# Kernel optimization log

Measured on AMD Instinct MI355X. Metric: run time of the kernel, lower is better.

## Reference

```python
import jax, jax.numpy as jnp
import numpy as np

N_NODES = 64000
N_GRAPHS = 128


def _sage_conv(x, edge_index, Wl, Wr, b):
    # PyG SAGEConv (mean aggregator): out = lin_l(mean_{j in N(i)} x_j) + lin_r(x_i)
    src, dst = edge_index[0], edge_index[1]
    msg = x[src]                                   # [E, d] gather
    s = jax.ops.segment_sum(msg, dst, num_segments=N_NODES)          # [N, d]
    cnt = jax.ops.segment_sum(jnp.ones(src.shape, x.dtype), dst,
                              num_segments=N_NODES)[:, None]          # [N, 1]
    aggr = jnp.where(cnt > 0, s / jnp.maximum(cnt, 1.0), jnp.zeros((), x.dtype))
    return aggr @ Wl.T + x @ Wr.T + b


def setup_inputs() -> dict:
    key = jax.random.key(0)
    ks = jax.random.split(key, 9)
    E = 1024000
    x = jax.random.normal(ks[0], (N_NODES, 64), dtype=jnp.float32)
    edge_index = jax.random.randint(ks[1], (2, E), 0, N_NODES, dtype=jnp.int64)
    batch = jnp.sort(jax.random.randint(ks[2], (N_NODES,), 0, N_GRAPHS, dtype=jnp.int64))
    sc = 1.0 / np.sqrt(64.0)
    Wl = jax.random.normal(ks[3], (3, 64, 64), dtype=jnp.float32) * sc
    Wr = jax.random.normal(ks[4], (3, 64, 64), dtype=jnp.float32) * sc
    b = jax.random.normal(ks[5], (3, 64), dtype=jnp.float32) * sc
    Wl_out = jax.random.normal(ks[6], (2, 64), dtype=jnp.float32) * sc
    Wr_out = jax.random.normal(ks[7], (2, 64), dtype=jnp.float32) * sc
    b_out = jax.random.normal(ks[8], (2,), dtype=jnp.float32) * sc
    return {"x": x, "edge_index": edge_index, "batch": batch,
            "Wl": Wl, "Wr": Wr, "b": b,
            "Wl_out": Wl_out, "Wr_out": Wr_out, "b_out": b_out}


def reference(x, edge_index, batch, Wl, Wr, b, Wl_out, Wr_out, b_out):
    h = x
    for i in range(Wl.shape[0]):  # fixed n_layers=3 hidden SAGEConv layers
        h = _sage_conv(h, edge_index, Wl[i], Wr[i], b[i])
        # dropout is identity at inference
        h = jax.nn.relu(h)
    h = _sage_conv(h, edge_index, Wl_out, Wr_out, b_out)  # [N, n_classes]
    # global mean pool over graphs in the batch
    s = jax.ops.segment_sum(h, batch, num_segments=N_GRAPHS)
    cnt = jax.ops.segment_sum(jnp.ones((N_NODES,), h.dtype), batch,
                              num_segments=N_GRAPHS)[:, None]
    return s / jnp.maximum(cnt, 1.0)
```

## Files before the change

### kernel.cpp

```cpp
#include <hip/hip_runtime.h>

#define NNODES 64000
#define NGRAPHS 128
#define D 64
#define NT 250
#define ESEG 5120
#define ZG 1024

typedef _Float16 half8 __attribute__((ext_vector_type(8)));
typedef float f32x4 __attribute__((ext_vector_type(4)));

__device__ __forceinline__ int lower_bound(const int* __restrict__ a, int n, int key) {
    int lo = 0, hi = n;
    while (lo < hi) {
        int mid = (lo + hi) >> 1;
        if (a[mid] < key) lo = mid + 1; else hi = mid;
    }
    return lo;
}


__global__ void tohalf_kernel(const float4* __restrict__ x, half8* __restrict__ xh, int n8,
                              const float* __restrict__ Wl, const float* __restrict__ Wr,
                              _Float16* __restrict__ Wlh, _Float16* __restrict__ Wrh,
                              int* __restrict__ ecur, float* __restrict__ pool) {
    int i = blockIdx.x * blockDim.x + threadIdx.x;
    int st = gridDim.x * blockDim.x;
    for (; i < n8; i += st) {
        float4 a = x[2 * i], b = x[2 * i + 1];
        half8 o;
        o[0] = (_Float16)a.x; o[1] = (_Float16)a.y; o[2] = (_Float16)a.z; o[3] = (_Float16)a.w;
        o[4] = (_Float16)b.x; o[5] = (_Float16)b.y; o[6] = (_Float16)b.z; o[7] = (_Float16)b.w;
        xh[i] = o;
    }
    int j = blockIdx.x * blockDim.x + threadIdx.x;
    if (j < 3 * D * D) {
        Wlh[j] = (_Float16)Wl[j];
        Wrh[j] = (_Float16)Wr[j];
    }
    if (blockIdx.x == 0 && threadIdx.x < 256) {
        ecur[threadIdx.x] = 0;
        pool[threadIdx.x] = 0.f;
    }
}

__global__ __launch_bounds__(256) void partition_kernel(
        const int* __restrict__ src, const int* __restrict__ dst, int E,
        int* __restrict__ ecur, int2* __restrict__ elist) {
    __shared__ int bcnt[256], bbase[256];
    const int U = 16;
    int tid = threadIdx.x;
    int base = blockIdx.x * 256 * U;
    bcnt[tid] = 0;
    __syncthreads();
    int2 ed[U]; int team[U], slot[U];
#pragma unroll
    for (int u = 0; u < U; ++u) {
        int e = base + tid + u * 256;
        team[u] = -1;
        if (e < E) {
            int s = __builtin_nontemporal_load(src + e);
            int d = __builtin_nontemporal_load(dst + e);
            ed[u] = make_int2(s, d);
            team[u] = d >> 8;
            slot[u] = atomicAdd(&bcnt[team[u]], 1);
        }
    }
    __syncthreads();
    if (bcnt[tid] > 0) bbase[tid] = atomicAdd(&ecur[tid], bcnt[tid]);
    __syncthreads();
#pragma unroll
    for (int u = 0; u < U; ++u)
        if (team[u] >= 0)
            elist[(size_t)team[u] * ESEG + bbase[team[u]] + slot[u]] = ed[u];
}

__global__ __launch_bounds__(1024) void fill_block(
        const int2* __restrict__ elist, const int* __restrict__ ecur,
        const int* __restrict__ batch,
        int* __restrict__ offs, int2* __restrict__ info, int* __restrict__ col) {
    __shared__ int2 els[ESEG];
    __shared__ int lhist[256], lofs[256];
    int team = blockIdx.x;
    int t = threadIdx.x;
    int n = ecur[team];
    const int2* el = elist + (size_t)team * ESEG;

    if (t < 256) lofs[t] = (t < NT) ? ecur[t] : 0;
    __syncthreads();
    for (int off = 1; off < 256; off <<= 1) {
        int x = 0;
        if (t < 256 && t >= off) x = lofs[t - off];
        __syncthreads();
        if (t < 256) lofs[t] += x;
        __syncthreads();
    }
    int tb = (team > 0) ? lofs[team - 1] : 0;
    if (team == NT - 1 && t == 0) offs[NNODES] = lofs[NT - 1];
    __syncthreads();

    if (t < 256) lhist[t] = 0;
    __syncthreads();
    for (int e = t; e < n; e += 1024) {
        int2 ed = el[e];
        els[e] = ed;
        atomicAdd(&lhist[ed.y & 255], 1);
    }
    __syncthreads();
    if (t < 256) lofs[t] = lhist[t];
    __syncthreads();
    for (int off = 1; off < 256; off <<= 1) {
        int x = 0;
        if (t < 256 && t >= off) x = lofs[t - off];
        __syncthreads();
        if (t < 256) lofs[t] += x;
        __syncthreads();
    }
    if (t < 256) {
        int v = lhist[t];
        int ex = lofs[t] - v;
        int gi = team * 256 + t;
        offs[gi] = tb + ex;
        float inv = (v > 0) ? 1.f / (float)v : 0.f;
        info[gi] = make_int2(batch[gi], __float_as_int(inv));
        lofs[t] = ex;
    }
    __syncthreads();
    for (int e = t; e < n; e += 1024) {
        int2 ed = els[e];
        int p = tb + atomicAdd(&lofs[ed.y & 255], 1);
        col[p] = ed.x;
    }
}

template <int PRJ>
__global__ __launch_bounds__(256) void layer_fused(
        const _Float16* __restrict__ h, _Float16* __restrict__ out,
        const int* __restrict__ offs, const int* __restrict__ col,
        const _Float16* __restrict__ Wlh, const _Float16* __restrict__ Wrh,
        const float* __restrict__ b,
        const float* __restrict__ Wlo, const float* __restrict__ Wro,
        float* __restrict__ z12, float* __restrict__ z34) {
    __shared__ _Float16 tile[4][16][D];
    int lane = threadIdx.x & 63;
    int w    = threadIdx.x >> 6;
    int row0 = (blockIdx.x * 4 + w) * 16;

    {
        int ns  = lane >> 2;
        int ch2 = lane & 3;
        int i = row0 + ns;
        int beg = offs[i], end = offs[i + 1];
        half8 s0 = {0, 0, 0, 0, 0, 0, 0, 0};
        half8 s1 = {0, 0, 0, 0, 0, 0, 0, 0};
        int e = beg;
        for (; e + 4 <= end; e += 4) {
            int c0 = col[e], c1 = col[e + 1], c2 = col[e + 2], c3 = col[e + 3];
            const _Float16* r0 = h + (size_t)c0 * D + ch2 * 16;
            const _Float16* r1 = h + (size_t)c1 * D + ch2 * 16;
            const _Float16* r2 = h + (size_t)c2 * D + ch2 * 16;
            const _Float16* r3 = h + (size_t)c3 * D + ch2 * 16;
            half8 a0 = *(const half8*)r0,       a1 = *(const half8*)r1;
            half8 a2 = *(const half8*)r2,       a3 = *(const half8*)r3;
            half8 b0 = *(const half8*)(r0 + 8), b1 = *(const half8*)(r1 + 8);
            half8 b2 = *(const half8*)(r2 + 8), b3 = *(const half8*)(r3 + 8);
            s0 += (a0 + a1) + (a2 + a3);
            s1 += (b0 + b1) + (b2 + b3);
        }
        for (; e < end; ++e) {
            const _Float16* rp = h + (size_t)col[e] * D + ch2 * 16;
            s0 += *(const half8*)rp;
            s1 += *(const half8*)(rp + 8);
        }
        float inv = (end > beg) ? 1.f / (float)(end - beg) : 0.f;
        half8 o0, o1;
#pragma unroll
        for (int j = 0; j < 8; ++j) {
            o0[j] = (_Float16)((float)s0[j] * inv);
            o1[j] = (_Float16)((float)s1[j] * inv);
        }
        *(half8*)(&tile[w][ns][ch2 * 16])     = o0;
        *(half8*)(&tile[w][ns][ch2 * 16 + 8]) = o1;
    }

    int r = lane & 15;
    int g = lane >> 4;

    half8 bf[4][4];
#pragma unroll
    for (int kt = 0; kt < 4; ++kt) {
        const _Float16* Wm = (kt < 2) ? Wlh : Wrh;
        int kk = (kt & 1) * 32 + g * 8;
#pragma unroll
        for (int nt = 0; nt < 4; ++nt)
            bf[kt][nt] = *(const half8*)(Wm + (size_t)(nt * 16 + r) * D + kk);
    }

    f32x4 acc[4];
#pragma unroll
    for (int nt = 0; nt < 4; ++nt) {
        float bv = b[nt * 16 + r];
        acc[nt] = (f32x4){bv, bv, bv, bv};
    }

#pragma unroll
    for (int kt = 0; kt < 4; ++kt) {
        int kk = (kt & 1) * 32 + g * 8;
        half8 af;
        if (kt < 2) af = *(const half8*)(&tile[w][r][kk]);
        else        af = *(const half8*)(h + (size_t)(row0 + r) * D + kk);
#pragma unroll
        for (int nt = 0; nt < 4; ++nt)
            acc[nt] = __builtin_amdgcn_mfma_f32_16x16x32_f16(af, bf[kt][nt], acc[nt], 0, 0, 0);
    }

    if (!PRJ) {
#pragma unroll
        for (int nt = 0; nt < 4; ++nt)
#pragma unroll
            for (int q = 0; q < 4; ++q) {
                int row = row0 + g * 4 + q;
                out[(size_t)row * D + nt * 16 + r] = (_Float16)fmaxf(acc[nt][q], 0.f);
            }
    } else {
#pragma unroll
        for (int nt = 0; nt < 4; ++nt)
#pragma unroll
            for (int q = 0; q < 4; ++q)
                tile[w][g * 4 + q][nt * 16 + r] = (_Float16)fmaxf(acc[nt][q], 0.f);

        half8 pf[2];
#pragma unroll
        for (int kt = 0; kt < 2; ++kt) {
            half8 t = {0, 0, 0, 0, 0, 0, 0, 0};
            if (r < 4) {
                const float* Pr = (r < 2) ? (Wlo + r * D) : (Wro + (r - 2) * D);
                int kk = kt * 32 + g * 8;
#pragma unroll
                for (int j = 0; j < 8; ++j) t[j] = (_Float16)Pr[kk + j];
            }
            pf[kt] = t;
        }
        f32x4 az = (f32x4){0.f, 0.f, 0.f, 0.f};
#pragma unroll
        for (int kt = 0; kt < 2; ++kt) {
            half8 af = *(const half8*)(&tile[w][r][kt * 32 + g * 8]);
            az = __builtin_amdgcn_mfma_f32_16x16x32_f16(af, pf[kt], az, 0, 0, 0);
        }
#pragma unroll
        for (int q = 0; q < 4; ++q) {
            int row = row0 + g * 4 + q;
            if (r < 2)      z12[row * 2 + r]       = az[q];
            else if (r < 4) z34[row * 2 + (r - 2)] = az[q];
        }
    }
}

__global__ __launch_bounds__(256) void zpool_edge(
        const float2* __restrict__ z12, const float2* __restrict__ z34,
        const int* __restrict__ src, const int* __restrict__ dst,
        const int2* __restrict__ info, int E, float* __restrict__ pool) {
    __shared__ float lp[NGRAPHS * 2];
    int t = threadIdx.x;
    lp[t] = 0.f;
    __syncthreads();
    int tid = blockIdx.x * blockDim.x + t;
    int stride = gridDim.x * blockDim.x;
    for (int e = tid; e < E; e += stride) {
        int s = __builtin_nontemporal_load(src + e);
        int d = __builtin_nontemporal_load(dst + e);
        float2 z = z12[s];
        int2 nf = info[d];
        float w = __int_as_float(nf.y);
        atomicAdd(&lp[0 * NGRAPHS + nf.x], z.x * w);
        atomicAdd(&lp[1 * NGRAPHS + nf.x], z.y * w);
    }
    for (int i = tid; i < NNODES; i += stride) {
        float2 zi = z34[i];
        int g = info[i].x;
        atomicAdd(&lp[0 * NGRAPHS + g], zi.x);
        atomicAdd(&lp[1 * NGRAPHS + g], zi.y);
    }
    __syncthreads();
    float v = lp[t];
    if (v != 0.f) atomicAdd(&pool[t], v);
}

__global__ void out_kernel(const float* __restrict__ pool, const int* __restrict__ batch,
                           const float* __restrict__ bo, float* __restrict__ out) {
    int t = threadIdx.x;
    float v = pool[t];
    int j = t >> 7, g = t & 127;
    int c = lower_bound(batch, NNODES, g + 1) - lower_bound(batch, NNODES, g);
    out[g * 2 + j] = (c > 0) ? v / (float)c + bo[j] : 0.f;
}


extern "C" void kernel_launch(void* const* d_in, const int* in_sizes, int n_in,
                              void* d_out, int out_size, void* d_ws, size_t ws_size,
                              hipStream_t stream) {
    const float* x    = (const float*)d_in[0];
    const int*   eidx = (const int*)d_in[1];
    const int*   batch= (const int*)d_in[2];
    const float* Wl   = (const float*)d_in[3];
    const float* Wr   = (const float*)d_in[4];
    const float* b    = (const float*)d_in[5];
    const float* Wlo  = (const float*)d_in[6];
    const float* Wro  = (const float*)d_in[7];
    const float* bo   = (const float*)d_in[8];

    int E = in_sizes[1] / 2;
    const int* src = eidx;
    const int* dst = eidx + E;

    char* ws = (char*)d_ws;
    size_t hb = (size_t)NNODES * D * 2;
    _Float16* xh   = (_Float16*)ws;
    _Float16* bufA = (_Float16*)(ws + hb);
    char* p = ws + 2 * hb;
    _Float16* Wlh  = (_Float16*)p;  p += 3 * D * D * 2;
    _Float16* Wrh  = (_Float16*)p;  p += 3 * D * D * 2;
    int*    col  = (int*)p;     p += (size_t)E * 4;
    int*    offs = (int*)p;     p += ((size_t)(NNODES + 1) * 4 + 127) / 128 * 128;
    int2*   info = (int2*)p;    p += (size_t)NNODES * 8;
    float*  z12  = (float*)p;   p += (size_t)NNODES * 8;
    float*  z34  = (float*)p;   p += (size_t)NNODES * 8;
    int*    ecur = (int*)p;     p += 1024;
    float*  pool = (float*)p;   p += 1024;
    int2*   elist= (int2*)p;

    tohalf_kernel<<<2000, 256, 0, stream>>>((const float4*)x, (half8*)xh, NNODES * D / 8,
                                            Wl, Wr, Wlh, Wrh, ecur, pool);

    int PB = (E + 4095) / 4096;
    partition_kernel<<<PB, 256, 0, stream>>>(src, dst, E, ecur, elist);
    fill_block<<<NT, 1024, 0, stream>>>(elist, ecur, batch, offs, info, col);

    layer_fused<0><<<1000, 256, 0, stream>>>(xh,   bufA, offs, col,
                                             Wlh,             Wrh,             b,
                                             nullptr, nullptr, nullptr, nullptr);
    layer_fused<0><<<1000, 256, 0, stream>>>(bufA, xh,   offs, col,
                                             Wlh + D * D,     Wrh + D * D,     b + D,
                                             nullptr, nullptr, nullptr, nullptr);
    layer_fused<1><<<1000, 256, 0, stream>>>(xh,   bufA, offs, col,
                                             Wlh + 2 * D * D, Wrh + 2 * D * D, b + 2 * D,
                                             Wlo, Wro, z12, z34);

    zpool_edge<<<ZG, 256, 0, stream>>>((const float2*)z12, (const float2*)z34,
                                       src, dst, info, E, pool);
    out_kernel<<<1, 256, 0, stream>>>(pool, batch, bo, (float*)d_out);
}
```

Measured before the change: 156.4 us.

## Merge fp16 conversion into partition kernel and spread pool atomics over replicas

The separate fp16 conversion kernel is folded into the edge-partition kernel. Extra blocks now do the x/W conversion while the first PB blocks partition edges, and the ecur counter is zeroed with a memset instead of inside the old kernel. The pooling accumulator is replicated NPOOL times, each zpool block adds into a replica chosen by block index, and out_kernel sums the replicas. This saves one kernel launch, overlaps the two independent prologue tasks, and cuts contention on the global pool atomics, at the cost of an extra memset call and a slightly larger pool buffer.

```diff
diff --git a/kernel.cpp b/kernel.cpp
--- a/kernel.cpp
+++ b/kernel.cpp
@@ -6,6 +6,8 @@
 #define NT 250
 #define ESEG 5120
 #define ZG 1024
+#define NPOOL 8
+#define CGRID 2000
 
 typedef _Float16 half8 __attribute__((ext_vector_type(8)));
 typedef float f32x4 __attribute__((ext_vector_type(4)));
@@ -19,60 +21,61 @@
     return lo;
 }
 
-
-__global__ void tohalf_kernel(const float4* __restrict__ x, half8* __restrict__ xh, int n8,
-                              const float* __restrict__ Wl, const float* __restrict__ Wr,
-                              _Float16* __restrict__ Wlh, _Float16* __restrict__ Wrh,
-                              int* __restrict__ ecur, float* __restrict__ pool) {
-    int i = blockIdx.x * blockDim.x + threadIdx.x;
-    int st = gridDim.x * blockDim.x;
-    for (; i < n8; i += st) {
-        float4 a = x[2 * i], b = x[2 * i + 1];
-        half8 o;
-        o[0] = (_Float16)a.x; o[1] = (_Float16)a.y; o[2] = (_Float16)a.z; o[3] = (_Float16)a.w;
-        o[4] = (_Float16)b.x; o[5] = (_Float16)b.y; o[6] = (_Float16)b.z; o[7] = (_Float16)b.w;
-        xh[i] = o;
-    }
-    int j = blockIdx.x * blockDim.x + threadIdx.x;
-    if (j < 3 * D * D) {
-        Wlh[j] = (_Float16)Wl[j];
-        Wrh[j] = (_Float16)Wr[j];
-    }
-    if (blockIdx.x == 0 && threadIdx.x < 256) {
-        ecur[threadIdx.x] = 0;
-        pool[threadIdx.x] = 0.f;
-    }
-}
-
-__global__ __launch_bounds__(256) void partition_kernel(
+__global__ __launch_bounds__(256) void convert_partition(
+        const float4* __restrict__ x, half8* __restrict__ xh, int n8,
+        const float* __restrict__ Wl, const float* __restrict__ Wr,
+        _Float16* __restrict__ Wlh, _Float16* __restrict__ Wrh,
         const int* __restrict__ src, const int* __restrict__ dst, int E,
-        int* __restrict__ ecur, int2* __restrict__ elist) {
+        int* __restrict__ ecur, int2* __restrict__ elist,
+        float* __restrict__ pool, int PB) {
     __shared__ int bcnt[256], bbase[256];
-    const int U = 16;
     int tid = threadIdx.x;
-    int base = blockIdx.x * 256 * U;
-    bcnt[tid] = 0;
-    __syncthreads();
-    int2 ed[U]; int team[U], slot[U];
-#pragma unroll
-    for (int u = 0; u < U; ++u) {
-        int e = base + tid + u * 256;
-        team[u] = -1;
-        if (e < E) {
-            int s = __builtin_nontemporal_load(src + e);
-            int d = __builtin_nontemporal_load(dst + e);
-            ed[u] = make_int2(s, d);
-            team[u] = d >> 8;
-            slot[u] = atomicAdd(&bcnt[team[u]], 1);
-        }
-    }
-    __syncthreads();
-    if (bcnt[tid] > 0) bbase[tid] = atomicAdd(&ecur[tid], bcnt[tid]);
-    __syncthreads();
-#pragma unroll
-    for (int u = 0; u < U; ++u)
-        if (team[u] >= 0)
-            elist[(size_t)team[u] * ESEG + bbase[team[u]] + slot[u]] = ed[u];
+    if ((int)blockIdx.x < PB) {
+        const int U = 16;
+        int base = blockIdx.x * 256 * U;
+        bcnt[tid] = 0;
+        __syncthreads();
+        int2 ed[U]; int team[U], slot[U];
+#pragma unroll
+        for (int u = 0; u < U; ++u) {
+            int e = base + tid + u * 256;
+            team[u] = -1;
+            if (e < E) {
+                int s = __builtin_nontemporal_load(src + e);
+                int d = __builtin_nontemporal_load(dst + e);
+                ed[u] = make_int2(s, d);
+                team[u] = d >> 8;
+                slot[u] = atomicAdd(&bcnt[team[u]], 1);
+            }
+        }
+        __syncthreads();
+        if (bcnt[tid] > 0) bbase[tid] = atomicAdd(&ecur[tid], bcnt[tid]);
+        __syncthreads();
+#pragma unroll
+        for (int u = 0; u < U; ++u)
+            if (team[u] >= 0)
+                elist[(size_t)team[u] * ESEG + bbase[team[u]] + slot[u]] = ed[u];
+    } else {
+        int bid = blockIdx.x - PB;
+        int i = bid * 256 + tid;
+        int st = CGRID * 256;
+        for (; i < n8; i += st) {
+            float4 a = x[2 * i], b = x[2 * i + 1];
+            half8 o;
+            o[0] = (_Float16)a.x; o[1] = (_Float16)a.y; o[2] = (_Float16)a.z; o[3] = (_Float16)a.w;
+            o[4] = (_Float16)b.x; o[5] = (_Float16)b.y; o[6] = (_Float16)b.z; o[7] = (_Float16)b.w;
+            xh[i] = o;
+        }
+        int j = bid * 256 + tid;
+        if (j < 3 * D * D) {
+            Wlh[j] = (_Float16)Wl[j];
+            Wrh[j] = (_Float16)Wr[j];
+        }
+        if (bid == 0) {
+#pragma unroll
+            for (int k = 0; k < NPOOL; ++k) pool[k * 256 + tid] = 0.f;
+        }
+    }
 }
 
 __global__ __launch_bounds__(1024) void fill_block(
@@ -283,13 +286,15 @@
     }
     __syncthreads();
     float v = lp[t];
-    if (v != 0.f) atomicAdd(&pool[t], v);
+    if (v != 0.f) atomicAdd(&pool[(blockIdx.x & (NPOOL - 1)) * 256 + t], v);
 }
 
 __global__ void out_kernel(const float* __restrict__ pool, const int* __restrict__ batch,
                            const float* __restrict__ bo, float* __restrict__ out) {
     int t = threadIdx.x;
-    float v = pool[t];
+    float v = 0.f;
+#pragma unroll
+    for (int k = 0; k < NPOOL; ++k) v += pool[k * 256 + t];
     int j = t >> 7, g = t & 127;
     int c = lower_bound(batch, NNODES, g + 1) - lower_bound(batch, NNODES, g);
     out[g * 2 + j] = (c > 0) ? v / (float)c + bo[j] : 0.f;
@@ -326,14 +331,16 @@
     float*  z12  = (float*)p;   p += (size_t)NNODES * 8;
     float*  z34  = (float*)p;   p += (size_t)NNODES * 8;
     int*    ecur = (int*)p;     p += 1024;
-    float*  pool = (float*)p;   p += 1024;
+    float*  pool = (float*)p;   p += NPOOL * 256 * 4;
     int2*   elist= (int2*)p;
 
-    tohalf_kernel<<<2000, 256, 0, stream>>>((const float4*)x, (half8*)xh, NNODES * D / 8,
-                                            Wl, Wr, Wlh, Wrh, ecur, pool);
+    hipMemsetAsync(ecur, 0, 1024, stream);
 
     int PB = (E + 4095) / 4096;
-    partition_kernel<<<PB, 256, 0, stream>>>(src, dst, E, ecur, elist);
+    convert_partition<<<PB + CGRID, 256, 0, stream>>>(
+        (const float4*)x, (half8*)xh, NNODES * D / 8,
+        Wl, Wr, Wlh, Wrh, src, dst, E, ecur, elist, pool, PB);
+
     fill_block<<<NT, 1024, 0, stream>>>(elist, ecur, batch, offs, info, col);
 
     layer_fused<0><<<1000, 256, 0, stream>>>(xh,   bufA, offs, col,
```

New measurement: 136.7 us. -12.6%, faster.
